# Kernel optimization log

Hardware: AMD Instinct MI355X
Metric: run time of the kernel (lower is better)

## Reference

```python
import jax, jax.numpy as jnp
import numpy as np

BIG_K, SMALL_K = 31, 5
C_OUT, GROUP_IN = 64, 4
NK = -(-BIG_K // SMALL_K)  # ceil = 7
C_IN = C_OUT * GROUP_IN * NK  # 1792
B, L = 8, 4096
# real_pad[i] = int((center - i) * small_kernel), center = (nk-1)/2
REAL_PAD = jnp.array([int(((NK - 1) / 2.0 - i) * SMALL_K) for i in range(NK)], dtype=jnp.int32)


def _shuffle_idx(rng):
    # per group: for each c_out, a random permutation of its nk channel slots
    groups = []
    for _ in range(GROUP_IN):
        groups.append(np.concatenate([rng.permutation(NK) + i * NK for i in range(C_OUT)]))
    return jnp.asarray(np.concatenate(groups), dtype=jnp.int32)


def _identity_idx(rng):
    groups = []
    for _ in range(GROUP_IN):
        g = rng.integers(0, NK, size=C_OUT) + np.arange(C_OUT) * NK
        groups.append(np.repeat(g, NK))
    return jnp.asarray(np.concatenate(groups), dtype=jnp.int32)


def setup_inputs() -> dict:
    key = jax.random.key(0)
    x = jax.random.normal(key, (B, C_IN, L), dtype=jnp.float32)
    rng = np.random.default_rng(123)
    return {
        "x": x,
        "shift_idx_1": _shuffle_idx(rng),
        "shift_idx_2": _shuffle_idx(rng),
        "shift_idx_3": _identity_idx(rng),
    }


def _shift_and_accumulate(x, shift_idx):
    # x: [B, C_IN, L]; per-channel zero-filled roll by REAL_PAD[idx % nk],
    # then sum channels sharing the same c_out slot.
    Bb, C, Ll = x.shape
    shifts = REAL_PAD[shift_idx % NK]            # [C]
    t = jnp.arange(Ll, dtype=jnp.int32)
    src = t[None, :] - shifts[:, None]           # [C, L] source positions
    valid = (src >= 0) & (src < Ll)              # zero-fill mask (roll + zeroing)
    src_c = jnp.clip(src, 0, Ll - 1)
    chan = jnp.arange(C, dtype=jnp.int32)[:, None]
    shifted = x[:, chan, src_c] * valid[None].astype(x.dtype)  # [B, C, L]
    # channel layout is [group_in, c_out, nk] -> reduce group_in and nk
    return shifted.reshape(Bb, GROUP_IN, C_OUT, NK, Ll).sum(axis=(1, 3))  # [B, c_out, L]


def reference(x, shift_idx_1, shift_idx_2, shift_idx_3):
    x1 = _shift_and_accumulate(x, shift_idx_1)
    x2 = _shift_and_accumulate(x, shift_idx_2)
    x3 = _shift_and_accumulate(x, shift_idx_3)
    return (x1, x2, x3)
```

## Files before the change

### kernel.cpp

```cpp
#include <hip/hip_runtime.h>

#define B_      8
#define C_OUT_  64
#define GROUPS_ 4
#define NK_     7
#define C_IN_   1792
#define L_      4096
#define NCH     28

#define T_TILE  256
#define HALO    16
#define ROW     (T_TILE + 2 * HALO)
#define NGRAN   (NCH * (ROW / 4))
#define NGRAN_P 2048


__global__ __launch_bounds__(256, 5)
void addshift_fused_kernel(const float* __restrict__ x,
                           const int*   __restrict__ s1,
                           const int*   __restrict__ s2,
                           const int*   __restrict__ s3,
                           float*       __restrict__ out)
{
    __shared__ float lx[NGRAN_P * 4];

    const int tid  = threadIdx.x;
    const int blk  = blockIdx.x;
    const int tile = blk & (L_ / T_TILE - 1);
    const int co   = (blk >> 4) & (C_OUT_ - 1);
    const int b    = blk >> 10;
    const int t0   = tile * T_TILE;

    const int base_b = b * (C_IN_ * L_);

    float4 v[8];
    bool   ok[8];
#pragma unroll
    for (int it = 0; it < 8; ++it) {
        const int gi  = it * 256 + tid;
        const int gic = gi > (NGRAN - 1) ? (NGRAN - 1) : gi;
        const int cl  = gic / (ROW / 4);
        const int j   = gic - cl * (ROW / 4);
        const int g   = cl / NK_;
        const int k   = cl - g * NK_;
        const int ch  = g * (C_OUT_ * NK_) + co * NK_ + k;
        const int e   = t0 - HALO + j * 4;
        ok[it] = (e >= 0) && (e <= L_ - 4);
        const int ec  = e < 0 ? 0 : (e > L_ - 4 ? L_ - 4 : e);
        v[it] = *(const float4*)(x + base_b + ch * L_ + ec);
    }
#pragma unroll
    for (int it = 0; it < 8; ++it) {
        if (!ok[it]) v[it] = make_float4(0.f, 0.f, 0.f, 0.f);
        *(float4*)&lx[(it * 256 + tid) * 4] = v[it];
    }
    __syncthreads();

    float acc1 = 0.f, acc2 = 0.f, acc3 = 0.f;
    const float* lbase = &lx[tid + 1];
#pragma unroll
    for (int g = 0; g < GROUPS_; ++g) {
#pragma unroll
        for (int k = 0; k < NK_; ++k) {
            const int cl = g * NK_ + k;
            const int ch = g * (C_OUT_ * NK_) + co * NK_ + k;
            const int m1 = s1[ch] % NK_;
            const int m2 = s2[ch] % NK_;
            const int m3 = s3[ch] % NK_;
            const float* row = lbase + cl * ROW;
            acc1 += row[5 * m1];
            acc2 += row[5 * m2];
            acc3 += row[5 * m3];
        }
    }

    const int opos = (b * C_OUT_ + co) * L_ + t0 + tid;
    out[opos]                        = acc1;
    out[B_ * C_OUT_ * L_ + opos]     = acc2;
    out[2 * B_ * C_OUT_ * L_ + opos] = acc3;
}

extern "C" void kernel_launch(void* const* d_in, const int* in_sizes, int n_in,
                              void* d_out, int out_size, void* d_ws, size_t ws_size,
                              hipStream_t stream) {
    const float* x  = (const float*)d_in[0];
    const int*   s1 = (const int*)d_in[1];
    const int*   s2 = (const int*)d_in[2];
    const int*   s3 = (const int*)d_in[3];
    float* out = (float*)d_out;

    const int n_blocks = B_ * C_OUT_ * (L_ / T_TILE);
    addshift_fused_kernel<<<dim3(n_blocks), dim3(256), 0, stream>>>(x, s1, s2, s3, out);
}
```

Measured before the change: 324.3 us.

## Load input tiles directly into LDS and double tile width per block

Input tiles are now copied global-to-LDS with global_load_lds, which bypasses the register staging, and only edge tiles get a separate zero-fill pass for the halo. The time tile grows from 256 to 512, so each thread computes two outputs and writes them as float2 stores, which halves the halo overhead relative to useful data. LDS use per block roughly doubles and launch bounds drop to 2 blocks per CU, which can reduce occupancy and latency hiding.

```diff
diff --git a/kernel.cpp b/kernel.cpp
--- a/kernel.cpp
+++ b/kernel.cpp
@@ -8,56 +8,74 @@
 #define L_      4096
 #define NCH     28
 
-#define T_TILE  256
+#define T_TILE  512
 #define HALO    16
 #define ROW     (T_TILE + 2 * HALO)
-#define NGRAN   (NCH * (ROW / 4))
-#define NGRAN_P 2048
+#define GPR     (ROW / 4)
+#define NGRAN   (NCH * GPR)
+#define NIT     15
+#define NGRAN_P (NIT * 256)
+#define NTILE   (L_ / T_TILE)
 
 
-__global__ __launch_bounds__(256, 5)
+__device__ __forceinline__ void gload_lds16(const float* g, float* l) {
+    __builtin_amdgcn_global_load_lds(
+        (const __attribute__((address_space(1))) void*)g,
+        (__attribute__((address_space(3))) void*)l,
+        16, 0, 0);
+}
+
+__global__ __launch_bounds__(256, 2)
 void addshift_fused_kernel(const float* __restrict__ x,
                            const int*   __restrict__ s1,
                            const int*   __restrict__ s2,
                            const int*   __restrict__ s3,
                            float*       __restrict__ out)
 {
-    __shared__ float lx[NGRAN_P * 4];
+    __shared__ __align__(16) float lx[NGRAN_P * 4];
 
     const int tid  = threadIdx.x;
     const int blk  = blockIdx.x;
-    const int tile = blk & (L_ / T_TILE - 1);
-    const int co   = (blk >> 4) & (C_OUT_ - 1);
-    const int b    = blk >> 10;
+    const int tile = blk & (NTILE - 1);
+    const int co   = (blk >> 3) & (C_OUT_ - 1);
+    const int b    = blk >> 9;
     const int t0   = tile * T_TILE;
 
     const int base_b = b * (C_IN_ * L_);
+    const int wbase  = tid & ~63;
 
-    float4 v[8];
-    bool   ok[8];
 #pragma unroll
-    for (int it = 0; it < 8; ++it) {
+    for (int it = 0; it < NIT; ++it) {
         const int gi  = it * 256 + tid;
         const int gic = gi > (NGRAN - 1) ? (NGRAN - 1) : gi;
-        const int cl  = gic / (ROW / 4);
-        const int j   = gic - cl * (ROW / 4);
+        const int cl  = gic / GPR;
+        const int j   = gic - cl * GPR;
         const int g   = cl / NK_;
         const int k   = cl - g * NK_;
         const int ch  = g * (C_OUT_ * NK_) + co * NK_ + k;
         const int e   = t0 - HALO + j * 4;
-        ok[it] = (e >= 0) && (e <= L_ - 4);
         const int ec  = e < 0 ? 0 : (e > L_ - 4 ? L_ - 4 : e);
-        v[it] = *(const float4*)(x + base_b + ch * L_ + ec);
-    }
-#pragma unroll
-    for (int it = 0; it < 8; ++it) {
-        if (!ok[it]) v[it] = make_float4(0.f, 0.f, 0.f, 0.f);
-        *(float4*)&lx[(it * 256 + tid) * 4] = v[it];
+        gload_lds16(x + base_b + ch * L_ + ec, &lx[(it * 256 + wbase) * 4]);
     }
     __syncthreads();
 
-    float acc1 = 0.f, acc2 = 0.f, acc3 = 0.f;
-    const float* lbase = &lx[tid + 1];
+    if (tile == 0 || tile == NTILE - 1) {
+#pragma unroll
+        for (int it = 0; it < NIT; ++it) {
+            const int gi = it * 256 + tid;
+            if (gi < NGRAN) {
+                const int cl = gi / GPR;
+                const int j  = gi - cl * GPR;
+                const int e  = t0 - HALO + j * 4;
+                if (e < 0 || e > L_ - 4)
+                    *(float4*)&lx[gi * 4] = make_float4(0.f, 0.f, 0.f, 0.f);
+            }
+        }
+        __syncthreads();
+    }
+
+    float a1 = 0.f, c1 = 0.f, a2 = 0.f, c2 = 0.f, a3 = 0.f, c3 = 0.f;
+    const int p = 2 * tid;
 #pragma unroll
     for (int g = 0; g < GROUPS_; ++g) {
 #pragma unroll
@@ -67,17 +85,17 @@
             const int m1 = s1[ch] % NK_;
             const int m2 = s2[ch] % NK_;
             const int m3 = s3[ch] % NK_;
-            const float* row = lbase + cl * ROW;
-            acc1 += row[5 * m1];
-            acc2 += row[5 * m2];
-            acc3 += row[5 * m3];
+            const float* r = &lx[cl * ROW + p + 1];
+            const float* r1 = r + 5 * m1;  a1 += r1[0];  c1 += r1[1];
+            const float* r2 = r + 5 * m2;  a2 += r2[0];  c2 += r2[1];
+            const float* r3 = r + 5 * m3;  a3 += r3[0];  c3 += r3[1];
         }
     }
 
-    const int opos = (b * C_OUT_ + co) * L_ + t0 + tid;
-    out[opos]                        = acc1;
-    out[B_ * C_OUT_ * L_ + opos]     = acc2;
-    out[2 * B_ * C_OUT_ * L_ + opos] = acc3;
+    const int opos = (b * C_OUT_ + co) * L_ + t0 + p;
+    *(float2*)&out[opos]                        = make_float2(a1, c1);
+    *(float2*)&out[B_ * C_OUT_ * L_ + opos]     = make_float2(a2, c2);
+    *(float2*)&out[2 * B_ * C_OUT_ * L_ + opos] = make_float2(a3, c3);
 }
 
 extern "C" void kernel_launch(void* const* d_in, const int* in_sizes, int n_in,
@@ -89,6 +107,6 @@
     const int*   s3 = (const int*)d_in[3];
     float* out = (float*)d_out;
 
-    const int n_blocks = B_ * C_OUT_ * (L_ / T_TILE);
+    const int n_blocks = B_ * C_OUT_ * NTILE;
     addshift_fused_kernel<<<dim3(n_blocks), dim3(256), 0, stream>>>(x, s1, s2, s3, out);
 }
```

After: 326.2 us. Within noise of the previous version (+0.6%).
